# Kernel optimization log

Hardware: AMD Instinct MI355X
Metric: run time of the kernel (lower is better)

Reference implementation:

```python
import jax, jax.numpy as jnp
import numpy as np

EMBED_DIM = 1024
NUM_HEADS = 16
HEAD_DIM = EMBED_DIM // NUM_HEADS
CHUNK_SIZE = 10
LEFT_CONTEXT = 25
RIGHT_CONTEXT = 0
NEG_INF = -1e30  # stands in for float('-inf') additive mask, safe under softmax


def chunk_attention_mask(seq_len: int) -> jnp.ndarray:
    """Vectorized version of the per-row Python loop mask builder.
    Row i may attend to: its own chunk [chunk_start, chunk_end), the left
    context [i-left_context, chunk_start), and the right context
    [chunk_end, i+right_context+1)."""
    i = jnp.arange(seq_len)[:, None]
    j = jnp.arange(seq_len)[None, :]
    chunk_start = (i // CHUNK_SIZE) * CHUNK_SIZE
    chunk_end = jnp.minimum(chunk_start + CHUNK_SIZE, seq_len)
    in_chunk = (j >= chunk_start) & (j < chunk_end)
    in_left = (j >= i - LEFT_CONTEXT) & (j < chunk_start)
    in_right = (j >= chunk_end) & (j < jnp.minimum(seq_len, i + RIGHT_CONTEXT + 1))
    allowed = in_chunk | in_left | in_right
    return jnp.where(allowed, 0.0, NEG_INF).astype(jnp.float32)


def setup_inputs() -> dict:
    key = jax.random.key(0)
    ks = jax.random.split(key, 9)
    B, S, E = 2, 2048, EMBED_DIM
    s = 1.0 / np.sqrt(E)
    return {
        "hidden_states": jax.random.normal(ks[0], (B, S, E), jnp.float32),
        "Wq": jax.random.normal(ks[1], (E, E), jnp.float32) * s,
        "bq": jax.random.normal(ks[2], (E,), jnp.float32) * 0.02,
        "Wk": jax.random.normal(ks[3], (E, E), jnp.float32) * s,
        "bk": jax.random.normal(ks[4], (E,), jnp.float32) * 0.02,
        "Wv": jax.random.normal(ks[5], (E, E), jnp.float32) * s,
        "bv": jax.random.normal(ks[6], (E,), jnp.float32) * 0.02,
        "Wo": jax.random.normal(ks[7], (E, E), jnp.float32) * s,
        "bo": jax.random.normal(ks[8], (E,), jnp.float32) * 0.02,
    }


def reference(hidden_states, Wq, bq, Wk, bk, Wv, bv, Wo, bo):
    B, S, E = hidden_states.shape
    H, D = NUM_HEADS, HEAD_DIM
    scaling = D ** -0.5

    def proj(x, W, b):  # nn.Linear: x @ W.T + b, then split heads -> [B,H,S,D]
        y = jnp.einsum('bse,fe->bsf', x, W) + b
        return y.reshape(B, S, H, D).transpose(0, 2, 1, 3)

    q = proj(hidden_states, Wq, bq) * scaling
    k = proj(hidden_states, Wk, bk)
    v = proj(hidden_states, Wv, bv)

    scores = jnp.einsum('bhsd,bhtd->bhst', q, k)  # [B,H,S,S]
    scores = scores + chunk_attention_mask(S)[None, None]
    probs = jax.nn.softmax(scores, axis=-1)
    out = jnp.einsum('bhst,bhtd->bhsd', probs, v)  # [B,H,S,D]
    out = out.transpose(0, 2, 1, 3).reshape(B, S, E)
    out = jnp.einsum('bse,fe->bsf', out, Wo) + bo
    return out
```

## Files before the change

### kernel.cpp

```cpp
#include <hip/hip_runtime.h>
#include <stdint.h>

typedef unsigned short u16;
typedef __attribute__((ext_vector_type(8))) short short8;
typedef __attribute__((ext_vector_type(4))) short short4v;
typedef __attribute__((ext_vector_type(4))) float f32x4;

#define AS1 __attribute__((address_space(1)))
#define AS3 __attribute__((address_space(3)))

__device__ __forceinline__ u16 f2bf(float f) {
  uint32_t x = __builtin_bit_cast(uint32_t, f);
  uint32_t r = (x + 0x7fffu + ((x >> 16) & 1u)) >> 16;
  return (u16)r;
}
__device__ __forceinline__ float bf2f(u16 u) {
  return __builtin_bit_cast(float, (uint32_t)u << 16);
}

__device__ __forceinline__ void conv8(const float* __restrict__ s, u16* __restrict__ d, float sc) {
  float4 a = *(const float4*)s;
  float4 b = *(const float4*)(s + 4);
  union { u16 u[8]; uint4 v; } pk;
  pk.u[0] = f2bf(a.x * sc); pk.u[1] = f2bf(a.y * sc); pk.u[2] = f2bf(a.z * sc); pk.u[3] = f2bf(a.w * sc);
  pk.u[4] = f2bf(b.x * sc); pk.u[5] = f2bf(b.y * sc); pk.u[6] = f2bf(b.z * sc); pk.u[7] = f2bf(b.w * sc);
  *(uint4*)d = pk.v;
}
__device__ __forceinline__ void copy8f(const float* __restrict__ s, float* __restrict__ d, float sc) {
  float4 a = *(const float4*)s;
  float4 b = *(const float4*)(s + 4);
  a.x *= sc; a.y *= sc; a.z *= sc; a.w *= sc;
  b.x *= sc; b.y *= sc; b.z *= sc; b.w *= sc;
  *(float4*)d = a; *(float4*)(d + 4) = b;
}

__global__ void pack_kernel(const float* __restrict__ X,
                            const float* __restrict__ Wq, const float* __restrict__ bq,
                            const float* __restrict__ Wk, const float* __restrict__ bk,
                            const float* __restrict__ Wv, const float* __restrict__ bv,
                            const float* __restrict__ Wo,
                            u16* __restrict__ Xbf, u16* __restrict__ Wcat,
                            u16* __restrict__ Wobf, float* __restrict__ bcat) {
  int t = blockIdx.x * blockDim.x + threadIdx.x;
  if (t < 524288) { conv8(X + (size_t)t * 8, Xbf + (size_t)t * 8, 1.f); return; }
  t -= 524288;
  if (t < 131072) { conv8(Wq + (size_t)t * 8, Wcat + (size_t)t * 8, 0.125f); return; }
  t -= 131072;
  if (t < 131072) { conv8(Wk + (size_t)t * 8, Wcat + 1048576 + (size_t)t * 8, 1.f); return; }
  t -= 131072;
  if (t < 131072) { conv8(Wv + (size_t)t * 8, Wcat + 2097152 + (size_t)t * 8, 1.f); return; }
  t -= 131072;
  if (t < 131072) { conv8(Wo + (size_t)t * 8, Wobf + (size_t)t * 8, 1.f); return; }
  t -= 131072;
  if (t < 128) { copy8f(bq + t * 8, bcat + t * 8, 0.125f); return; }
  t -= 128;
  if (t < 128) { copy8f(bk + t * 8, bcat + 1024 + t * 8, 1.f); return; }
  t -= 128;
  if (t < 128) { copy8f(bv + t * 8, bcat + 2048 + t * 8, 1.f); return; }
}

template <bool OUT_BF16>
__global__ __launch_bounds__(256)
void gemm_bt(const u16* __restrict__ A, const u16* __restrict__ Bt,
             const float* __restrict__ bias, u16* __restrict__ Cbf,
             float* __restrict__ Cf, int M, int N, int K) {
  __shared__ u16 As[128 * 32];
  __shared__ u16 Bs[128 * 32];
  const int wv = threadIdx.x >> 6;
  const int lane = threadIdx.x & 63;
  const int bm = blockIdx.x, bn = blockIdx.y;
  const int wm = wv >> 1, wn = wv & 1;
  const int lrow = lane & 15, quad = lane >> 4;

  f32x4 acc[4][4];
#pragma unroll
  for (int i = 0; i < 4; ++i)
#pragma unroll
    for (int j = 0; j < 4; ++j) acc[i][j] = (f32x4){0.f, 0.f, 0.f, 0.f};

  const long arow = (long)bm * 128;
  const long brow = (long)bn * 128;
  const int srow = lane >> 2;
  const int scol = ((lane & 3) ^ ((lane >> 3) & 3)) * 8;
  const int swz = (quad ^ ((lrow >> 1) & 3)) * 8;

  for (int k0 = 0; k0 < K; k0 += 32) {
    __syncthreads();
#pragma unroll
    for (int it = 0; it < 2; ++it) {
      const int s = wv * 2 + it;
      const int r = s * 16 + srow;
      const u16* ga = A + (arow + r) * K + k0 + scol;
      const u16* gb = Bt + (brow + r) * K + k0 + scol;
      u16* la = (u16*)As + s * 512;
      u16* lb = (u16*)Bs + s * 512;
      __builtin_amdgcn_global_load_lds((AS1 void*)ga, (AS3 void*)la, 16, 0, 0);
      __builtin_amdgcn_global_load_lds((AS1 void*)gb, (AS3 void*)lb, 16, 0, 0);
    }
    __syncthreads();

    short8 af[4], bfr[4];
#pragma unroll
    for (int mi = 0; mi < 4; ++mi)
      af[mi] = *(const short8*)(As + (wm * 64 + mi * 16 + lrow) * 32 + swz);
#pragma unroll
    for (int ni = 0; ni < 4; ++ni)
      bfr[ni] = *(const short8*)(Bs + (wn * 64 + ni * 16 + lrow) * 32 + swz);
#pragma unroll
    for (int mi = 0; mi < 4; ++mi)
#pragma unroll
      for (int ni = 0; ni < 4; ++ni)
        acc[mi][ni] = __builtin_amdgcn_mfma_f32_16x16x32_bf16(af[mi], bfr[ni], acc[mi][ni], 0, 0, 0);
  }

#pragma unroll
  for (int mi = 0; mi < 4; ++mi) {
#pragma unroll
    for (int ni = 0; ni < 4; ++ni) {
      const int col = bn * 128 + wn * 64 + ni * 16 + lrow;
      const float bv = bias[col];
#pragma unroll
      for (int r = 0; r < 4; ++r) {
        const int row = bm * 128 + wm * 64 + mi * 16 + quad * 4 + r;
        const float v = acc[mi][ni][r] + bv;
        if constexpr (OUT_BF16) Cbf[(long)row * N + col] = f2bf(v);
        else Cf[(long)row * N + col] = v;
      }
    }
  }
}

#define NCH 205
#define VT_STRIDE 68
#define PB_STRIDE 72
#define WAVE_LDS (64 * VT_STRIDE + 16 * PB_STRIDE)

__global__ __launch_bounds__(256)
void attn_kernel(const u16* __restrict__ QKV, u16* __restrict__ ctx) {
  __shared__ __align__(16) u16 lds[4 * WAVE_LDS];
  const int wv = threadIdx.x >> 6;
  const int lane = threadIdx.x & 63;
  u16* Vt = lds + wv * WAVE_LDS;
  u16* Pb = Vt + 64 * VT_STRIDE;

  const int n = lane & 15, quad = lane >> 4;

  const int gw = blockIdx.x * 4 + wv;
  const int b = gw / (16 * NCH);
  int rem = gw - b * 16 * NCH;
  const int h = rem / NCH;
  const int c = rem - h * NCH;
  const int cs = c * 10;
  const int nq = min(10, 2048 - cs);
  const int w0 = max(cs - 25, 0);
  const int L = cs + nq - w0;

  const long base = ((long)b * 2048) * 3072 + (long)h * 64;

  for (int idx = lane; idx < (64 * VT_STRIDE) / 8; idx += 64)
    *(uint4*)(Vt + idx * 8) = (uint4){0, 0, 0, 0};
  for (int idx = lane; idx < (16 * PB_STRIDE) / 8; idx += 64)
    *(uint4*)(Pb + idx * 8) = (uint4){0, 0, 0, 0};

  for (int j = 0; j < L; ++j)
    Vt[lane * VT_STRIDE + j] = QKV[base + (long)(w0 + j) * 3072 + 2048 + lane];

  const int mclamp = min(n, nq - 1);
  const long qrow = base + (long)(cs + mclamp) * 3072;
  short8 aq0 = *(const short8*)(QKV + qrow + quad * 8);
  short8 aq1 = *(const short8*)(QKV + qrow + 32 + quad * 8);

  f32x4 sc[3];
#pragma unroll
  for (int t = 0; t < 3; ++t) {
    const int jj = min(16 * t + n, L - 1);
    const long krow = base + (long)(w0 + jj) * 3072 + 1024;
    short8 bk0 = *(const short8*)(QKV + krow + quad * 8);
    short8 bk1 = *(const short8*)(QKV + krow + 32 + quad * 8);
    f32x4 z = (f32x4){0.f, 0.f, 0.f, 0.f};
    z = __builtin_amdgcn_mfma_f32_16x16x32_bf16(aq0, bk0, z, 0, 0, 0);
    sc[t] = __builtin_amdgcn_mfma_f32_16x16x32_bf16(aq1, bk1, z, 0, 0, 0);
  }

#pragma unroll
  for (int r = 0; r < 4; ++r) {
    const int i = cs + quad * 4 + r;
    const int jlo = max(i - 25, 0) - w0;
    float v0 = (n >= jlo && n < L)      ? sc[0][r] : -1e30f;
    float v1 = (16 + n >= jlo && 16 + n < L) ? sc[1][r] : -1e30f;
    float v2 = (32 + n >= jlo && 32 + n < L) ? sc[2][r] : -1e30f;
    float m = fmaxf(v0, fmaxf(v1, v2));
#pragma unroll
    for (int off = 8; off > 0; off >>= 1) m = fmaxf(m, __shfl_xor(m, off));
    float p0 = __expf(v0 - m), p1 = __expf(v1 - m), p2 = __expf(v2 - m);
    float sum = p0 + p1 + p2;
#pragma unroll
    for (int off = 8; off > 0; off >>= 1) sum += __shfl_xor(sum, off);
    const float inv = 1.f / sum;
    u16* prow = Pb + (quad * 4 + r) * PB_STRIDE;
    prow[n]      = f2bf(p0 * inv);
    prow[16 + n] = f2bf(p1 * inv);
    prow[32 + n] = f2bf(p2 * inv);
  }

  short8 ap0 = *(const short8*)(Pb + n * PB_STRIDE + quad * 8);
  short8 ap1 = *(const short8*)(Pb + n * PB_STRIDE + 32 + quad * 8);
  f32x4 o[4];
#pragma unroll
  for (int dt = 0; dt < 4; ++dt) {
    const u16* vrow = Vt + (dt * 16 + n) * VT_STRIDE;
    short4v l0 = *(const short4v*)(vrow + quad * 8);
    short4v h0 = *(const short4v*)(vrow + quad * 8 + 4);
    short4v l1 = *(const short4v*)(vrow + 32 + quad * 8);
    short4v h1 = *(const short4v*)(vrow + 32 + quad * 8 + 4);
    short8 bv0 = __builtin_shufflevector(l0, h0, 0, 1, 2, 3, 4, 5, 6, 7);
    short8 bv1 = __builtin_shufflevector(l1, h1, 0, 1, 2, 3, 4, 5, 6, 7);
    f32x4 z = (f32x4){0.f, 0.f, 0.f, 0.f};
    z = __builtin_amdgcn_mfma_f32_16x16x32_bf16(ap0, bv0, z, 0, 0, 0);
    o[dt] = __builtin_amdgcn_mfma_f32_16x16x32_bf16(ap1, bv1, z, 0, 0, 0);
  }

#pragma unroll
  for (int dt = 0; dt < 4; ++dt) {
#pragma unroll
    for (int r = 0; r < 4; ++r) {
      const int row = quad * 4 + r;
      if (row < nq)
        ctx[((long)b * 2048 + cs + row) * 1024 + h * 64 + dt * 16 + n] = f2bf(o[dt][r]);
    }
  }
}

extern "C" void kernel_launch(void* const* d_in, const int* in_sizes, int n_in,
                              void* d_out, int out_size, void* d_ws, size_t ws_size,
                              hipStream_t stream) {
  const float* X  = (const float*)d_in[0];
  const float* Wq = (const float*)d_in[1];
  const float* bq = (const float*)d_in[2];
  const float* Wk = (const float*)d_in[3];
  const float* bk = (const float*)d_in[4];
  const float* Wv = (const float*)d_in[5];
  const float* bv = (const float*)d_in[6];
  const float* Wo = (const float*)d_in[7];
  const float* bo = (const float*)d_in[8];
  float* out = (float*)d_out;

  char* ws = (char*)d_ws;
  u16* Xbf   = (u16*)(ws);
  u16* Wcat  = (u16*)(ws + 8388608);
  u16* Wobf  = (u16*)(ws + 14680064);
  float* bcat = (float*)(ws + 16777216);
  u16* QKV   = (u16*)(ws + 16789504);
  u16* ctx   = (u16*)(ws + 41955328);

  pack_kernel<<<4098, 256, 0, stream>>>(X, Wq, bq, Wk, bk, Wv, bv, Wo, Xbf, Wcat, Wobf, bcat);
  gemm_bt<true ><<<dim3(32, 24), 256, 0, stream>>>(Xbf, Wcat, bcat, QKV, nullptr, 4096, 3072, 1024);
  attn_kernel<<<1640, 256, 0, stream>>>(QKV, ctx);
  gemm_bt<false><<<dim3(32, 8), 256, 0, stream>>>(ctx, Wobf, bo, nullptr, out, 4096, 1024, 1024);
}
```

Measured before the change: 173.9 us.

## Double-buffer LDS tiles in GEMM and use narrower N tile for output projection

The bf16 GEMM now keeps two LDS buffers for the A and B tiles. It issues the async global-to-LDS loads for the next K slice before running the MFMAs on the current one, which drops one barrier per iteration and overlaps memory latency with compute. The kernel is also templated on the N tile width. The output projection uses BN=64, which doubles its grid to 512 blocks so more CUs are kept busy. The cost is twice the LDS per block, and the 64-wide tile does fewer MFMAs per A fragment load, so data reuse drops.

```diff
diff --git a/kernel.cpp b/kernel.cpp
--- a/kernel.cpp
+++ b/kernel.cpp
@@ -59,65 +59,78 @@
   if (t < 128) { copy8f(bv + t * 8, bcat + 2048 + t * 8, 1.f); return; }
 }
 
-template <bool OUT_BF16>
+template <int BN, bool OUT_BF16>
 __global__ __launch_bounds__(256)
 void gemm_bt(const u16* __restrict__ A, const u16* __restrict__ Bt,
              const float* __restrict__ bias, u16* __restrict__ Cbf,
              float* __restrict__ Cf, int M, int N, int K) {
-  __shared__ u16 As[128 * 32];
-  __shared__ u16 Bs[128 * 32];
+  constexpr int SEG_A = 8;
+  constexpr int SEG_B = BN / 16;
+  constexpr int NSEG = SEG_A + SEG_B;
+  constexpr int NI = BN / 32;
+  __shared__ u16 As[2][128 * 32];
+  __shared__ u16 Bs[2][BN * 32];
   const int wv = threadIdx.x >> 6;
   const int lane = threadIdx.x & 63;
   const int bm = blockIdx.x, bn = blockIdx.y;
   const int wm = wv >> 1, wn = wv & 1;
   const int lrow = lane & 15, quad = lane >> 4;
 
-  f32x4 acc[4][4];
+  f32x4 acc[4][NI];
 #pragma unroll
   for (int i = 0; i < 4; ++i)
 #pragma unroll
-    for (int j = 0; j < 4; ++j) acc[i][j] = (f32x4){0.f, 0.f, 0.f, 0.f};
+    for (int j = 0; j < NI; ++j) acc[i][j] = (f32x4){0.f, 0.f, 0.f, 0.f};
 
   const long arow = (long)bm * 128;
-  const long brow = (long)bn * 128;
+  const long brow = (long)bn * BN;
   const int srow = lane >> 2;
   const int scol = ((lane & 3) ^ ((lane >> 3) & 3)) * 8;
   const int swz = (quad ^ ((lrow >> 1) & 3)) * 8;
 
+  auto stage = [&](int nb, int k0) {
+#pragma unroll
+    for (int it = 0; it < NSEG / 4; ++it) {
+      const int s = wv * (NSEG / 4) + it;
+      const u16* g;
+      u16* l;
+      if (s < SEG_A) {
+        g = A + (arow + s * 16 + srow) * K + k0 + scol;
+        l = (u16*)As[nb] + s * 512;
+      } else {
+        g = Bt + (brow + (s - SEG_A) * 16 + srow) * K + k0 + scol;
+        l = (u16*)Bs[nb] + (s - SEG_A) * 512;
+      }
+      __builtin_amdgcn_global_load_lds((AS1 void*)g, (AS3 void*)l, 16, 0, 0);
+    }
+  };
+
+  stage(0, 0);
+  int cur = 0;
   for (int k0 = 0; k0 < K; k0 += 32) {
     __syncthreads();
-#pragma unroll
-    for (int it = 0; it < 2; ++it) {
-      const int s = wv * 2 + it;
-      const int r = s * 16 + srow;
-      const u16* ga = A + (arow + r) * K + k0 + scol;
-      const u16* gb = Bt + (brow + r) * K + k0 + scol;
-      u16* la = (u16*)As + s * 512;
-      u16* lb = (u16*)Bs + s * 512;
-      __builtin_amdgcn_global_load_lds((AS1 void*)ga, (AS3 void*)la, 16, 0, 0);
-      __builtin_amdgcn_global_load_lds((AS1 void*)gb, (AS3 void*)lb, 16, 0, 0);
-    }
-    __syncthreads();
-
-    short8 af[4], bfr[4];
+    if (k0 + 32 < K) stage(cur ^ 1, k0 + 32);
+
+    short8 af[4], bfr[NI];
 #pragma unroll
     for (int mi = 0; mi < 4; ++mi)
-      af[mi] = *(const short8*)(As + (wm * 64 + mi * 16 + lrow) * 32 + swz);
-#pragma unroll
-    for (int ni = 0; ni < 4; ++ni)
-      bfr[ni] = *(const short8*)(Bs + (wn * 64 + ni * 16 + lrow) * 32 + swz);
+      af[mi] = *(const short8*)(As[cur] + (wm * 64 + mi * 16 + lrow) * 32 + swz);
+#pragma unroll
+    for (int ni = 0; ni < NI; ++ni)
+      bfr[ni] = *(const short8*)(Bs[cur] + (wn * (BN / 2) + ni * 16 + lrow) * 32 + swz);
 #pragma unroll
     for (int mi = 0; mi < 4; ++mi)
 #pragma unroll
-      for (int ni = 0; ni < 4; ++ni)
+      for (int ni = 0; ni < NI; ++ni)
         acc[mi][ni] = __builtin_amdgcn_mfma_f32_16x16x32_bf16(af[mi], bfr[ni], acc[mi][ni], 0, 0, 0);
+    cur ^= 1;
   }
 
 #pragma unroll
   for (int mi = 0; mi < 4; ++mi) {
 #pragma unroll
-    for (int ni = 0; ni < 4; ++ni) {
-      const int col = bn * 128 + wn * 64 + ni * 16 + lrow;
+    for (int ni = 0; ni < NI; ++ni) {
+      const int col = bn * BN + wn * (BN / 2) + ni * 16 + lrow;
       const float bv = bias[col];
 #pragma unroll
       for (int r = 0; r < 4; ++r) {
@@ -254,7 +267,7 @@
   u16* ctx   = (u16*)(ws + 41955328);
 
   pack_kernel<<<4098, 256, 0, stream>>>(X, Wq, bq, Wk, bk, Wv, bv, Wo, Xbf, Wcat, Wobf, bcat);
-  gemm_bt<true ><<<dim3(32, 24), 256, 0, stream>>>(Xbf, Wcat, bcat, QKV, nullptr, 4096, 3072, 1024);
+  gemm_bt<128, true ><<<dim3(32, 24), 256, 0, stream>>>(Xbf, Wcat, bcat, QKV, nullptr, 4096, 3072, 1024);
   attn_kernel<<<1640, 256, 0, stream>>>(QKV, ctx);
-  gemm_bt<false><<<dim3(32, 8), 256, 0, stream>>>(ctx, Wobf, bo, nullptr, out, 4096, 1024, 1024);
-}
+  gemm_bt<64, false><<<dim3(32, 16), 256, 0, stream>>>(ctx, Wobf, bo, nullptr, out, 4096, 1024, 1024);
+}
```

Result: faster. 163.0 us (-6.3%).
